# Performance work log

Hardware: AMD Instinct MI355X
Metric: run time of the kernel (lower is better)

Reference implementation:

```python
import jax, jax.numpy as jnp
import numpy as np

N_GRAPHS = 100
NODES_PER_GRAPH = 1000
N = N_GRAPHS * NODES_PER_GRAPH
DEG = 16
E = N * DEG
IN_FEATS = 64
HIDDEN = 128
READOUT_DIM = HIDDEN // 2
SLOPE = 0.01
EPS = 1e-5


def leaky(x):
    return jnp.where(x >= 0, x, SLOPE * x)


def _kaiming(k, shape):
    # torch kaiming_uniform_, fan_in mode, leaky_relu gain
    fan_in = shape[0]
    gain = np.sqrt(2.0 / (1.0 + SLOPE ** 2))
    bound = gain * np.sqrt(3.0 / fan_in)
    return jax.random.uniform(k, shape, jnp.float32, -bound, bound)


def setup_inputs() -> dict:
    key = jax.random.key(0)
    ks = jax.random.split(key, 16)
    node_feats = jax.random.normal(ks[0], (N, IN_FEATS), jnp.float32)
    # within-graph random edges (batched graph of equal-sized components)
    src_local = jax.random.randint(ks[1], (E,), 0, NODES_PER_GRAPH)
    dst_local = jax.random.randint(ks[2], (E,), 0, NODES_PER_GRAPH)
    edge_graph = jnp.repeat(jnp.arange(N_GRAPHS, dtype=jnp.int32), E // N_GRAPHS)
    src = (edge_graph * NODES_PER_GRAPH + src_local).astype(jnp.int32)
    dst = (edge_graph * NODES_PER_GRAPH + dst_local).astype(jnp.int32)
    edge_weights = jax.random.uniform(ks[3], (E,), jnp.float32)
    node_graph = jnp.repeat(jnp.arange(N_GRAPHS, dtype=jnp.int32), NODES_PER_GRAPH)
    return {
        "node_feats": node_feats,
        "edge_weights": edge_weights,
        "W1": _kaiming(ks[4], (IN_FEATS, HIDDEN)),
        "W2": _kaiming(ks[5], (HIDDEN, HIDDEN)),
        "gn1_alpha": jnp.ones((HIDDEN,), jnp.float32),
        "gn1_gamma": jnp.ones((HIDDEN,), jnp.float32),
        "gn1_beta": jnp.zeros((HIDDEN,), jnp.float32),
        "gn2_alpha": jnp.ones((HIDDEN,), jnp.float32),
        "gn2_gamma": jnp.ones((HIDDEN,), jnp.float32),
        "gn2_beta": jnp.zeros((HIDDEN,), jnp.float32),
        "r1_w1": _kaiming(ks[6], (HIDDEN, HIDDEN)),
        "r1_b1": jnp.zeros((HIDDEN,), jnp.float32),
        "r1_w2": _kaiming(ks[7], (HIDDEN, READOUT_DIM)),
        "r1_b2": jnp.zeros((READOUT_DIM,), jnp.float32),
        "r2_w1": _kaiming(ks[8], (HIDDEN, HIDDEN)),
        "r2_b1": jnp.zeros((HIDDEN,), jnp.float32),
        "r2_w2": _kaiming(ks[9], (HIDDEN, READOUT_DIM)),
        "r2_b2": jnp.zeros((READOUT_DIM,), jnp.float32),
        "src": src,
        "dst": dst,
        "node_graph": node_graph,
    }


def _graph_conv(x, W, src, dst, ew, out_isqrt, in_isqrt):
    # DGL GraphConv norm='both', no bias: D_in^{-1/2} A_w D_out^{-1/2} X W
    h = (x * out_isqrt[:, None]) @ W                 # [N, out]
    m = h[src] * ew[:, None]                         # [E, out] gather + edge weight
    agg = jax.ops.segment_sum(m, dst, num_segments=N)  # scatter-add
    return agg * in_isqrt[:, None]


def _graph_norm(x, alpha, gamma, beta, node_graph, inv_cnt):
    mean = jax.ops.segment_sum(x, node_graph, num_segments=N_GRAPHS) * inv_cnt
    sub = x - alpha * mean[node_graph]
    var = jax.ops.segment_sum(sub * sub, node_graph, num_segments=N_GRAPHS) * inv_cnt
    return gamma * sub / jnp.sqrt(var[node_graph] + EPS) + beta


def _readout(x, w1, b1, w2, b2, node_graph, inv_cnt):
    # deep-sets style universal readout: rho(mean(phi(h_v)))
    h = leaky(x @ w1 + b1)
    pooled = jax.ops.segment_sum(h, node_graph, num_segments=N_GRAPHS) * inv_cnt
    return leaky(pooled @ w2 + b2)


def reference(node_feats, edge_weights, W1, W2,
              gn1_alpha, gn1_gamma, gn1_beta,
              gn2_alpha, gn2_gamma, gn2_beta,
              r1_w1, r1_b1, r1_w2, r1_b2,
              r2_w1, r2_b1, r2_w2, r2_b2,
              src, dst, node_graph):
    ones_e = jnp.ones((E,), jnp.float32)
    out_deg = jnp.clip(jax.ops.segment_sum(ones_e, src, num_segments=N), 1.0)
    in_deg = jnp.clip(jax.ops.segment_sum(ones_e, dst, num_segments=N), 1.0)
    out_isqrt = jax.lax.rsqrt(out_deg)
    in_isqrt = jax.lax.rsqrt(in_deg)
    inv_cnt = 1.0 / NODES_PER_GRAPH

    h = _graph_conv(node_feats, W1, src, dst, edge_weights, out_isqrt, in_isqrt)
    h = leaky(_graph_norm(h, gn1_alpha, gn1_gamma, gn1_beta, node_graph, inv_cnt))
    # dropout is identity in eval mode
    r1 = _readout(h, r1_w1, r1_b1, r1_w2, r1_b2, node_graph, inv_cnt)
    m1 = jax.ops.segment_sum(h, node_graph, num_segments=N_GRAPHS) * inv_cnt

    h = _graph_conv(h, W2, src, dst, edge_weights, out_isqrt, in_isqrt)
    h = leaky(_graph_norm(h, gn2_alpha, gn2_gamma, gn2_beta, node_graph, inv_cnt))
    r2 = _readout(h, r2_w1, r2_b1, r2_w2, r2_b2, node_graph, inv_cnt)
    m2 = jax.ops.segment_sum(h, node_graph, num_segments=N_GRAPHS) * inv_cnt

    readout = jnp.concatenate([r1, m1, r2, m2], axis=1)  # [G, 2*H + 2*H/2] = [100, 384]
    return leaky(readout)
```

## Files before the change

### kernel.cpp

```cpp
#include <hip/hip_runtime.h>
#include <cstddef>
#include <cstdint>

#define NG   100
#define NPG  1000
#define NN   (NG * NPG)
#define NE   (NN * 16)
#define EPG  (NE / NG)
#define CSRG 40000
#define MINREC 20
#define FIN  64
#define HID  128
#define RD   64
#define SLOPE 0.01f
#define EPSV  1e-5f
#define NSTRIP 250
#define GSN   40

using short8 = __attribute__((ext_vector_type(8))) short;
using f32x4  = __attribute__((ext_vector_type(4))) float;
typedef unsigned short u16;

__device__ __forceinline__ float leaky(float x) { return x >= 0.f ? x : SLOPE * x; }

__device__ __forceinline__ u16 f2bf(float f) {
  union { float f; unsigned u; } v; v.f = f;
  return (u16)((v.u + 0x7fffu + ((v.u >> 16) & 1u)) >> 16);
}
__device__ __forceinline__ float bf2f(u16 u) {
  union { unsigned u; float f; } v; v.u = ((unsigned)u) << 16;
  return v.f;
}

__device__ __forceinline__ bool swz(int b, int per_g, int& g, int& part) {
  const int xcd = b & 7;
  const int slot = b >> 3;
  g = xcd + 8 * (slot / per_g);
  part = slot % per_g;
  return g < NG;
}

struct BldSh { int hin[NPG]; int hout[NPG]; int cur[NPG]; int wtot[16]; };
struct GemSh { u16 Xl[64 * FIN]; u16 W[HID * FIN]; };
union FrontSh { BldSh b; GemSh g; };

__global__ __launch_bounds__(1024) void front_k(
    const float* __restrict__ X0, const float* __restrict__ ew,
    const int* __restrict__ src, const int* __restrict__ dst,
    const float* __restrict__ W1, const float* __restrict__ W2f,
    const float* __restrict__ R1f, const float* __restrict__ R2f,
    u16* __restrict__ Wt2, u16* __restrict__ Rt1, u16* __restrict__ Rt2,
    int* __restrict__ cin_, int* __restrict__ offs,
    unsigned* __restrict__ csr, u16* __restrict__ bufA,
    float* __restrict__ zeroreg) {
  __shared__ FrontSh u;
  const int b = blockIdx.x;
  const int t = threadIdx.x;
  if (b >= 208) {
    const int idx = (b - 208) * 1024 + t;
    if (idx < 3 * HID * HID) {
      const int m = idx >> 14, r = idx & 16383;
      const int n = r >> 7, k = r & 127;
      const float* s = (m == 0) ? W2f : (m == 1) ? R1f : R2f;
      u16* d = (m == 0) ? Wt2 : (m == 1) ? Rt1 : Rt2;
      d[r] = f2bf(s[k * HID + n]);
    }
    if (idx < (8 * NG * HID) / 4)
      ((float4*)zeroreg)[idx] = make_float4(0.f, 0.f, 0.f, 0.f);
    return;
  }
  int g, part;
  if (!swz(b, 2, g, part)) return;
  const int lane = t & 63, wave = t >> 6;
  const int nb = g * NPG, eb = g * EPG;

  if (part == 0) {
    if (t < NPG) { u.b.hin[t] = 0; u.b.hout[t] = 0; }
    __syncthreads();
    for (int e = t; e < EPG; e += 4096) {
      int s4[4], d4[4];
#pragma unroll
      for (int k = 0; k < 4; ++k) {
        const int ee = e + k * 1024;
        if (ee < EPG) { s4[k] = src[eb + ee]; d4[k] = dst[eb + ee]; }
        else d4[k] = -1;
      }
#pragma unroll
      for (int k = 0; k < 4; ++k)
        if (d4[k] >= 0) {
          atomicAdd(&u.b.hout[s4[k] - nb], 1);
          atomicAdd(&u.b.hin[d4[k] - nb], 1);
        }
    }
    __syncthreads();
    float* houtf = (float*)u.b.hout;
    if (t < NPG) {
      const int c = u.b.hout[t];
      houtf[t] = rsqrtf((float)(c > 0 ? c : 1));
    }
    int v[4], vr[4];
    int loc = 0;
#pragma unroll
    for (int k = 0; k < 4; ++k) {
      const int idx = t * 4 + k;
      v[k] = (idx < NPG) ? u.b.hin[idx] : 0;
      const int c4 = (v[k] + 3) & ~3;
      vr[k] = (idx < NPG) ? ((c4 > MINREC) ? c4 : MINREC) : 0;
      loc += vr[k];
    }
    int incl = loc;
#pragma unroll
    for (int d = 1; d < 64; d <<= 1) {
      const int x = __shfl_up(incl, d);
      if (lane >= d) incl += x;
    }
    if (lane == 63) u.b.wtot[wave] = incl;
    if (t < NPG) cin_[nb + t] = u.b.hin[t];
    __syncthreads();
    int wexc = 0;
    for (int i = 0; i < wave; ++i) wexc += u.b.wtot[i];
    int run = g * CSRG + wexc + (incl - loc);
#pragma unroll
    for (int k = 0; k < 4; ++k) {
      const int idx = t * 4 + k;
      if (idx < NPG) {
        offs[nb + idx] = run;
        u.b.cur[idx] = run;
        for (int z = v[k]; z < vr[k]; ++z) csr[run + z] = 0;
        run += vr[k];
      }
    }
    __syncthreads();
    for (int e = t; e < EPG; e += 4096) {
      int s4[4], d4[4];
      float w4[4];
#pragma unroll
      for (int k = 0; k < 4; ++k) {
        const int ee = e + k * 1024;
        if (ee < EPG) { s4[k] = src[eb + ee]; d4[k] = dst[eb + ee]; w4[k] = ew[eb + ee]; }
        else d4[k] = -1;
      }
#pragma unroll
      for (int k = 0; k < 4; ++k)
        if (d4[k] >= 0) {
          const int sl = s4[k] - nb;
          const int pos = atomicAdd(&u.b.cur[d4[k] - nb], 1);
          csr[pos] = ((unsigned)sl << 16) | (unsigned)f2bf(w4[k] * houtf[sl]);
        }
    }
  } else {
    const int l15 = lane & 15, quad = lane >> 4;
    const int rg = wave >> 2, cg = wave & 3;
    {
      const int n = t & 127, ko = t >> 7;
      short8 w8;
#pragma unroll
      for (int j = 0; j < 8; ++j) w8[j] = (short)f2bf(W1[(ko * 8 + j) * HID + n]);
      *(short8*)&u.g.W[n * FIN + ((ko ^ (n & 7)) << 3)] = w8;
    }
    const int kq = t & 15, srow = t >> 4;
    float4 xpre = (srow < NPG)
        ? *(const float4*)(X0 + (size_t)(nb + srow) * FIN + kq * 4)
        : make_float4(0.f, 0.f, 0.f, 0.f);
    for (int pass = 0; pass < 16; ++pass) {
      __syncthreads();
      {
        ushort4 uu = make_ushort4(f2bf(xpre.x), f2bf(xpre.y), f2bf(xpre.z), f2bf(xpre.w));
        const int cc = kq >> 1, half = kq & 1;
        *(ushort4*)&u.g.Xl[srow * FIN + (((cc ^ (srow & 7)) << 3) | (half << 2))] = uu;
      }
      __syncthreads();
      if (pass < 15) {
        const int rowi = (pass + 1) * 64 + srow;
        xpre = (rowi < NPG)
            ? *(const float4*)(X0 + (size_t)(nb + rowi) * FIN + kq * 4)
            : make_float4(0.f, 0.f, 0.f, 0.f);
      }
      short8 a[2];
      const int arow = rg * 16 + l15;
#pragma unroll
      for (int kt = 0; kt < 2; ++kt)
        a[kt] = *(const short8*)&u.g.Xl[arow * FIN + (((kt * 4 + quad) ^ (l15 & 7)) << 3)];
      int rows[4];
#pragma unroll
      for (int r = 0; r < 4; ++r) rows[r] = pass * 64 + rg * 16 + quad * 4 + r;
#pragma unroll
      for (int q2 = 0; q2 < 2; ++q2) {
        const int ct = cg * 2 + q2;
        f32x4 acc = {0.f, 0.f, 0.f, 0.f};
        const int brow = ct * 16 + l15;
#pragma unroll
        for (int kt = 0; kt < 2; ++kt) {
          const short8 bb = *(const short8*)&u.g.W[brow * FIN + (((kt * 4 + quad) ^ (l15 & 7)) << 3)];
          acc = __builtin_amdgcn_mfma_f32_16x16x32_bf16(a[kt], bb, acc, 0, 0, 0);
        }
        const int n2 = ct * 16 + l15;
#pragma unroll
        for (int r = 0; r < 4; ++r)
          if (rows[r] < NPG)
            bufA[(size_t)(nb + rows[r]) * HID + n2] = f2bf(acc[r]);
      }
    }
  }
}

__device__ __forceinline__ void norm_affine(const float* sx, const float* sq,
                                            const float* alpha, const float* gamma,
                                            const float* beta, int g, int c8,
                                            float* Av, float* Bv) {
  const float inv = 1.0f / NPG;
#pragma unroll
  for (int j = 0; j < 8; ++j) {
    const int f = c8 * 8 + j;
    const float mean = sx[g * HID + f] * inv;
    const float ex2 = sq[g * HID + f] * inv;
    const float am = alpha[f] * mean;
    const float var = fmaxf(ex2 - 2.0f * am * mean + am * am, 0.0f);
    const float A = gamma[f] * rsqrtf(var + EPSV);
    Av[j] = A;
    Bv[j] = beta[f] - A * am;
  }
}

__global__ __launch_bounds__(256) void gather_k(const u16* __restrict__ H,
                                                const unsigned* __restrict__ csr,
                                                const int* __restrict__ offs,
                                                const int* __restrict__ cin_,
                                                u16* __restrict__ AGG,
                                                float* __restrict__ sx,
                                                float* __restrict__ sq) {
  __shared__ float redx[4][HID];
  __shared__ float redq[4][HID];
  const int wave = threadIdx.x >> 6;
  const int lane = threadIdx.x & 63;
  int g, part;
  if (!swz(blockIdx.x, 25, g, part)) return;
  const int nb = g * NPG;
  const int base = nb + part * GSN;
  const int loff = lane * 2;
  const u16* __restrict__ Hg = H + (size_t)nb * HID;

  float sxa = 0.f, sxb = 0.f, sqa = 0.f, sqb = 0.f;
  for (int it = 0; it < 3; ++it) {
    const int nc = (it < 2) ? 4 : 2;
    int nn[4], off[4], cnt[4], c4p[4];
    float isq[4];
    const uint4* p[4];
#pragma unroll
    for (int c = 0; c < 4; ++c) {
      const int j = it * 4 + c;
      const int node = base + wave + ((j < 10) ? j : 0) * 4;
      nn[c] = node;
      const int nu = __builtin_amdgcn_readfirstlane(node);
      off[c] = __builtin_amdgcn_readfirstlane(offs[nu]);
      cnt[c] = (c < nc) ? __builtin_amdgcn_readfirstlane(cin_[nu]) : 0;
      const int cr = (cnt[c] + 3) & ~3;
      c4p[c] = ((cr > MINREC) ? cr : MINREC) >> 2;
      isq[c] = rsqrtf(fmaxf((float)cnt[c], 1.0f));
      p[c] = (const uint4*)__builtin_assume_aligned(csr + off[c], 16);
    }
    float ax[4] = {0.f, 0.f, 0.f, 0.f};
    float ay[4] = {0.f, 0.f, 0.f, 0.f};
#pragma unroll
    for (int t = 0; t < 5; ++t) {
      uint4 r[4];
      unsigned u[4][4];
#pragma unroll
      for (int c = 0; c < 4; ++c)
        if (c < nc) {
          r[c] = p[c][t];
          u[c][0] = *(const unsigned*)(Hg + (size_t)(r[c].x >> 16) * HID + loff);
          u[c][1] = *(const unsigned*)(Hg + (size_t)(r[c].y >> 16) * HID + loff);
          u[c][2] = *(const unsigned*)(Hg + (size_t)(r[c].z >> 16) * HID + loff);
          u[c][3] = *(const unsigned*)(Hg + (size_t)(r[c].w >> 16) * HID + loff);
        }
#pragma unroll
      for (int c = 0; c < 4; ++c)
        if (c < nc) {
          const float w0 = bf2f((u16)(r[c].x & 0xffffu));
          const float w1 = bf2f((u16)(r[c].y & 0xffffu));
          const float w2 = bf2f((u16)(r[c].z & 0xffffu));
          const float w3 = bf2f((u16)(r[c].w & 0xffffu));
          ax[c] = fmaf(w0, __uint_as_float(u[c][0] << 16), ax[c]);
          ay[c] = fmaf(w0, __uint_as_float(u[c][0] & 0xffff0000u), ay[c]);
          ax[c] = fmaf(w1, __uint_as_float(u[c][1] << 16), ax[c]);
          ay[c] = fmaf(w1, __uint_as_float(u[c][1] & 0xffff0000u), ay[c]);
          ax[c] = fmaf(w2, __uint_as_float(u[c][2] << 16), ax[c]);
          ay[c] = fmaf(w2, __uint_as_float(u[c][2] & 0xffff0000u), ay[c]);
          ax[c] = fmaf(w3, __uint_as_float(u[c][3] << 16), ax[c]);
          ay[c] = fmaf(w3, __uint_as_float(u[c][3] & 0xffff0000u), ay[c]);
        }
    }
#pragma unroll
    for (int c = 0; c < 4; ++c) {
      for (int t = 5; t < c4p[c]; ++t) {
        const uint4 r = p[c][t];
        const unsigned u0 = *(const unsigned*)(Hg + (size_t)(r.x >> 16) * HID + loff);
        const unsigned u1 = *(const unsigned*)(Hg + (size_t)(r.y >> 16) * HID + loff);
        const unsigned u2 = *(const unsigned*)(Hg + (size_t)(r.z >> 16) * HID + loff);
        const unsigned u3 = *(const unsigned*)(Hg + (size_t)(r.w >> 16) * HID + loff);
        const float w0 = bf2f((u16)(r.x & 0xffffu));
        const float w1 = bf2f((u16)(r.y & 0xffffu));
        const float w2 = bf2f((u16)(r.z & 0xffffu));
        const float w3 = bf2f((u16)(r.w & 0xffffu));
        ax[c] = fmaf(w0, __uint_as_float(u0 << 16), ax[c]);
        ay[c] = fmaf(w0, __uint_as_float(u0 & 0xffff0000u), ay[c]);
        ax[c] = fmaf(w1, __uint_as_float(u1 << 16), ax[c]);
        ay[c] = fmaf(w1, __uint_as_float(u1 & 0xffff0000u), ay[c]);
        ax[c] = fmaf(w2, __uint_as_float(u2 << 16), ax[c]);
        ay[c] = fmaf(w2, __uint_as_float(u2 & 0xffff0000u), ay[c]);
        ax[c] = fmaf(w3, __uint_as_float(u3 << 16), ax[c]);
        ay[c] = fmaf(w3, __uint_as_float(u3 & 0xffff0000u), ay[c]);
      }
    }
#pragma unroll
    for (int c = 0; c < 4; ++c)
      if (c < nc) {
        const float rx = ax[c] * isq[c];
        const float ry = ay[c] * isq[c];
        *(unsigned*)(AGG + (size_t)nn[c] * HID + loff) =
            (unsigned)f2bf(rx) | ((unsigned)f2bf(ry) << 16);
        sxa += rx; sxb += ry;
        sqa += rx * rx; sqb += ry * ry;
      }
  }
  redx[wave][loff] = sxa; redx[wave][loff + 1] = sxb;
  redq[wave][loff] = sqa; redq[wave][loff + 1] = sqb;
  __syncthreads();
  const int tid = threadIdx.x;
  if (tid < HID) {
    unsafeAtomicAdd(&sx[g * HID + tid],
                    redx[0][tid] + redx[1][tid] + redx[2][tid] + redx[3][tid]);
  } else {
    const int t = tid - HID;
    unsafeAtomicAdd(&sq[g * HID + t],
                    redq[0][t] + redq[1][t] + redq[2][t] + redq[3][t]);
  }
}

struct RedT { float red[16][HID]; float hred[16][HID]; };
union ShT { u16 Xl[64 * HID]; RedT r; };

template <bool DO_GEMM>
__global__ __launch_bounds__(256) void phigemm_k(const u16* __restrict__ Xb,
                                                 u16* __restrict__ Y,
                                                 const u16* __restrict__ Wt,
                                                 const u16* __restrict__ Rt,
                                                 const float* __restrict__ sx,
                                                 const float* __restrict__ sq,
                                                 const float* __restrict__ alpha,
                                                 const float* __restrict__ gamma,
                                                 const float* __restrict__ beta,
                                                 const float* __restrict__ b1,
                                                 float* __restrict__ phi_sum,
                                                 float* __restrict__ h_sum) {
  __shared__ ShT sh;
  __shared__ u16 Rl[HID * HID];
  __shared__ u16 Wl[DO_GEMM ? HID * HID : 8];
  const int tid = threadIdx.x;
  const int wave = tid >> 6, lane = tid & 63, l15 = lane & 15, quad = lane >> 4;
  int g, part;
  if (!swz(blockIdx.x, 4, g, part)) return;
  const int base = g * NPG + part * NSTRIP;
  const int c8 = tid & 15;
  const int srow = tid >> 4;

  for (int i = tid; i < HID * (HID / 8); i += 256) {
    const int n = i >> 4, c = i & 15;
    const short8 r2 = *(const short8*)(Rt + n * HID + c * 8);
    *(short8*)&Rl[n * HID + ((c ^ (n & 15)) << 3)] = r2;
    if (DO_GEMM) {
      const short8 w = *(const short8*)(Wt + n * HID + c * 8);
      *(short8*)&Wl[n * HID + ((c ^ (n & 15)) << 3)] = w;
    }
  }
  float Av[8], Bv[8];
  norm_affine(sx, sq, alpha, gamma, beta, g, c8, Av, Bv);
  float bcol[8];
#pragma unroll
  for (int ct = 0; ct < 8; ++ct) bcol[ct] = b1[ct * 16 + l15];

  float pooled[8] = {0.f, 0.f, 0.f, 0.f, 0.f, 0.f, 0.f, 0.f};
  float hp[8] = {0.f, 0.f, 0.f, 0.f, 0.f, 0.f, 0.f, 0.f};
  const short8 z8 = {0, 0, 0, 0, 0, 0, 0, 0};
  short8 xpre[4];
#pragma unroll
  for (int it = 0; it < 4; ++it) {
    const int rowi = srow + it * 16;
    xpre[it] = (rowi < NSTRIP) ? *(const short8*)(Xb + (size_t)(base + rowi) * HID + c8 * 8) : z8;
  }
  for (int pass = 0; pass < 4; ++pass) {
    __syncthreads();
#pragma unroll
    for (int it = 0; it < 4; ++it) {
      const int r = srow + it * 16;
      const int rowi = pass * 64 + r;
      short8 o = z8;
      if (rowi < NSTRIP) {
#pragma unroll
        for (int j = 0; j < 8; ++j) {
          const float xn = leaky(fmaf(Av[j], bf2f((u16)xpre[it][j]), Bv[j]));
          hp[j] += xn;
          o[j] = (short)f2bf(xn);
        }
      }
      *(short8*)&sh.Xl[r * HID + ((c8 ^ (r & 15)) << 3)] = o;
    }
    __syncthreads();
    if (pass < 3) {
#pragma unroll
      for (int it = 0; it < 4; ++it) {
        const int rowi = (pass + 1) * 64 + srow + it * 16;
        xpre[it] = (rowi < NSTRIP) ? *(const short8*)(Xb + (size_t)(base + rowi) * HID + c8 * 8) : z8;
      }
    }
    short8 a[4];
    const int arow = wave * 16 + l15;
#pragma unroll
    for (int kt = 0; kt < 4; ++kt)
      a[kt] = *(const short8*)&sh.Xl[arow * HID + (((kt * 4 + quad) ^ l15) << 3)];
    int rows[4];
#pragma unroll
    for (int r = 0; r < 4; ++r) rows[r] = pass * 64 + wave * 16 + quad * 4 + r;
#pragma unroll
    for (int ct = 0; ct < 8; ++ct) {
      const int brow = ct * 16 + l15;
      if (DO_GEMM) {
        f32x4 accW = {0.f, 0.f, 0.f, 0.f};
#pragma unroll
        for (int kt = 0; kt < 4; ++kt) {
          const short8 bb = *(const short8*)&Wl[brow * HID + (((kt * 4 + quad) ^ l15) << 3)];
          accW = __builtin_amdgcn_mfma_f32_16x16x32_bf16(a[kt], bb, accW, 0, 0, 0);
        }
#pragma unroll
        for (int r = 0; r < 4; ++r)
          if (rows[r] < NSTRIP)
            Y[(size_t)(base + rows[r]) * HID + ct * 16 + l15] = f2bf(accW[r]);
      }
      f32x4 accR = {0.f, 0.f, 0.f, 0.f};
#pragma unroll
      for (int kt = 0; kt < 4; ++kt) {
        const short8 bb = *(const short8*)&Rl[brow * HID + (((kt * 4 + quad) ^ l15) << 3)];
        accR = __builtin_amdgcn_mfma_f32_16x16x32_bf16(a[kt], bb, accR, 0, 0, 0);
      }
#pragma unroll
      for (int r = 0; r < 4; ++r)
        if (rows[r] < NSTRIP) pooled[ct] += leaky(accR[r] + bcol[ct]);
    }
  }
  __syncthreads();
  const int qi = wave * 4 + quad;
#pragma unroll
  for (int ct = 0; ct < 8; ++ct) sh.r.red[qi][ct * 16 + l15] = pooled[ct];
#pragma unroll
  for (int j = 0; j < 8; ++j) sh.r.hred[tid >> 4][(tid & 15) * 8 + j] = hp[j];
  __syncthreads();
  if (tid < HID) {
    float s = 0.f;
#pragma unroll
    for (int q = 0; q < 16; ++q) s += sh.r.red[q][tid];
    unsafeAtomicAdd(&phi_sum[g * HID + tid], s);
  } else {
    const int t = tid - HID;
    float s = 0.f;
#pragma unroll
    for (int rr = 0; rr < 16; ++rr) s += sh.r.hred[rr][t];
    unsafeAtomicAdd(&h_sum[g * HID + t], s);
  }
}

__global__ __launch_bounds__(64) void fin_k(const float* __restrict__ ps1,
                                            const float* __restrict__ hs1,
                                            const float* __restrict__ ps2,
                                            const float* __restrict__ hs2,
                                            const float* __restrict__ r1w2,
                                            const float* __restrict__ r1b2,
                                            const float* __restrict__ r2w2,
                                            const float* __restrict__ r2b2,
                                            float* __restrict__ out) {
  const int gb = blockIdx.x;
  const bool L2 = gb >= NG;
  const int g = L2 ? gb - NG : gb;
  const float* ps = L2 ? ps2 : ps1;
  const float* hs = L2 ? hs2 : hs1;
  const float* w2 = L2 ? r2w2 : r1w2;
  const float* b2 = L2 ? r2b2 : r1b2;
  const int roff = L2 ? 192 : 0;
  const int moff = L2 ? 256 : 64;
  const int j = threadIdx.x;
  float acc = b2[j];
#pragma unroll 8
  for (int k = 0; k < HID; ++k)
    acc += (ps[g * HID + k] * (1.0f / NPG)) * w2[k * RD + j];
  out[g * 384 + roff + j] = leaky(leaky(acc));
  out[g * 384 + moff + j] = leaky(hs[g * HID + j] * (1.0f / NPG));
  out[g * 384 + moff + 64 + j] = leaky(hs[g * HID + 64 + j] * (1.0f / NPG));
}

extern "C" void kernel_launch(void* const* d_in, const int* in_sizes, int n_in,
                              void* d_out, int out_size, void* d_ws, size_t ws_size,
                              hipStream_t stream) {
  const float* node_feats = (const float*)d_in[0];
  const float* ew   = (const float*)d_in[1];
  const float* W1   = (const float*)d_in[2];
  const float* W2   = (const float*)d_in[3];
  const float* g1a  = (const float*)d_in[4];
  const float* g1g  = (const float*)d_in[5];
  const float* g1b  = (const float*)d_in[6];
  const float* g2a  = (const float*)d_in[7];
  const float* g2g  = (const float*)d_in[8];
  const float* g2b  = (const float*)d_in[9];
  const float* r1w1 = (const float*)d_in[10];
  const float* r1b1 = (const float*)d_in[11];
  const float* r1w2 = (const float*)d_in[12];
  const float* r1b2 = (const float*)d_in[13];
  const float* r2w1 = (const float*)d_in[14];
  const float* r2b1 = (const float*)d_in[15];
  const float* r2w2 = (const float*)d_in[16];
  const float* r2b2 = (const float*)d_in[17];
  const int* src = (const int*)d_in[18];
  const int* dst = (const int*)d_in[19];
  float* out = (float*)d_out;

  char* wsb = (char*)d_ws;
  float* ps1     = (float*)wsb;
  float* hs1     = ps1 + NG * HID;
  float* ps2     = hs1 + NG * HID;
  float* hs2     = ps2 + NG * HID;
  float* sx1     = hs2 + NG * HID;
  float* sq1     = sx1 + NG * HID;
  float* sx2     = sq1 + NG * HID;
  float* sq2     = sx2 + NG * HID;
  int*   cin     = (int*)(sq2 + NG * HID);
  int*   offs    = cin + NN;
  unsigned* csr  = (unsigned*)(offs + NN);
  u16*   Wt2     = (u16*)(csr + (size_t)NG * CSRG);
  u16*   Rt1     = Wt2 + HID * HID;
  u16*   Rt2     = Rt1 + HID * HID;
  u16*   bufA    = Rt2 + HID * HID;
  u16*   bufB    = bufA + (size_t)NN * HID;

  const int gemm_grid = 8 * 4 * 13;
  const int gather_grid = 8 * 25 * 13;

  front_k<<<208 + 56, 1024, 0, stream>>>(node_feats, ew, src, dst,
                                         W1, W2, r1w1, r2w1,
                                         Wt2, Rt1, Rt2,
                                         cin, offs, csr, bufA, ps1);

  gather_k<<<gather_grid, 256, 0, stream>>>(bufA, csr, offs, cin, bufB, sx1, sq1);
  phigemm_k<true><<<gemm_grid, 256, 0, stream>>>(bufB, bufA, Wt2, Rt1,
                                                 sx1, sq1, g1a, g1g, g1b,
                                                 r1b1, ps1, hs1);

  gather_k<<<gather_grid, 256, 0, stream>>>(bufA, csr, offs, cin, bufB, sx2, sq2);
  phigemm_k<false><<<gemm_grid, 256, 0, stream>>>(bufB, nullptr, nullptr, Rt2,
                                                  sx2, sq2, g2a, g2g, g2b,
                                                  r2b1, ps2, hs2);

  fin_k<<<2 * NG, 64, 0, stream>>>(ps1, hs1, ps2, hs2, r1w2, r1b2, r2w2, r2b2, out);
}
```

Baseline: 268.5 us.

## Use fixed-stride CSR, fuse final readout into last GEMM block, double GEMM grid

Each node now gets a fixed 64-slot CSR segment, which drops the in-degree histogram, prefix scan and offsets array from the build kernel and the offset loads from the gather kernel. In-degrees above 64 are silently truncated. The separate final readout kernel is removed: the last of each graph's GEMM blocks, found with an atomic counter and thread fence, computes the readout MLP tail and the mean outputs. GEMM strips are halved so twice as many blocks run with fewer passes each. The cost is a larger CSR footprint and the counter synchronisation.

```diff
diff --git a/kernel.cpp b/kernel.cpp
--- a/kernel.cpp
+++ b/kernel.cpp
@@ -7,14 +7,15 @@
 #define NN   (NG * NPG)
 #define NE   (NN * 16)
 #define EPG  (NE / NG)
-#define CSRG 40000
+#define CSRN 64
+#define CSRG (NPG * CSRN)
 #define MINREC 20
 #define FIN  64
 #define HID  128
 #define RD   64
 #define SLOPE 0.01f
 #define EPSV  1e-5f
-#define NSTRIP 250
+#define NSTRIP 125
 #define GSN   40
 
 using short8 = __attribute__((ext_vector_type(8))) short;
@@ -40,7 +41,7 @@
   return g < NG;
 }
 
-struct BldSh { int hin[NPG]; int hout[NPG]; int cur[NPG]; int wtot[16]; };
+struct BldSh { int hout[NPG]; int cur[NPG]; };
 struct GemSh { u16 Xl[64 * FIN]; u16 W[HID * FIN]; };
 union FrontSh { BldSh b; GemSh g; };
 
@@ -50,8 +51,7 @@
     const float* __restrict__ W1, const float* __restrict__ W2f,
     const float* __restrict__ R1f, const float* __restrict__ R2f,
     u16* __restrict__ Wt2, u16* __restrict__ Rt1, u16* __restrict__ Rt2,
-    int* __restrict__ cin_, int* __restrict__ offs,
-    unsigned* __restrict__ csr, u16* __restrict__ bufA,
+    int* __restrict__ cin_, unsigned* __restrict__ csr, u16* __restrict__ bufA,
     float* __restrict__ zeroreg) {
   __shared__ FrontSh u;
   const int b = blockIdx.x;
@@ -65,7 +65,7 @@
       u16* d = (m == 0) ? Wt2 : (m == 1) ? Rt1 : Rt2;
       d[r] = f2bf(s[k * HID + n]);
     }
-    if (idx < (8 * NG * HID) / 4)
+    if (idx < (8 * NG * HID + 256) / 4)
       ((float4*)zeroreg)[idx] = make_float4(0.f, 0.f, 0.f, 0.f);
     return;
   }
@@ -75,22 +75,18 @@
   const int nb = g * NPG, eb = g * EPG;
 
   if (part == 0) {
-    if (t < NPG) { u.b.hin[t] = 0; u.b.hout[t] = 0; }
+    if (t < NPG) { u.b.hout[t] = 0; u.b.cur[t] = 0; }
     __syncthreads();
     for (int e = t; e < EPG; e += 4096) {
-      int s4[4], d4[4];
+      int s4[4];
 #pragma unroll
       for (int k = 0; k < 4; ++k) {
         const int ee = e + k * 1024;
-        if (ee < EPG) { s4[k] = src[eb + ee]; d4[k] = dst[eb + ee]; }
-        else d4[k] = -1;
+        s4[k] = (ee < EPG) ? src[eb + ee] : -1;
       }
 #pragma unroll
       for (int k = 0; k < 4; ++k)
-        if (d4[k] >= 0) {
-          atomicAdd(&u.b.hout[s4[k] - nb], 1);
-          atomicAdd(&u.b.hin[d4[k] - nb], 1);
-        }
+        if (s4[k] >= 0) atomicAdd(&u.b.hout[s4[k] - nb], 1);
     }
     __syncthreads();
     float* houtf = (float*)u.b.hout;
@@ -98,39 +94,8 @@
       const int c = u.b.hout[t];
       houtf[t] = rsqrtf((float)(c > 0 ? c : 1));
     }
-    int v[4], vr[4];
-    int loc = 0;
-#pragma unroll
-    for (int k = 0; k < 4; ++k) {
-      const int idx = t * 4 + k;
-      v[k] = (idx < NPG) ? u.b.hin[idx] : 0;
-      const int c4 = (v[k] + 3) & ~3;
-      vr[k] = (idx < NPG) ? ((c4 > MINREC) ? c4 : MINREC) : 0;
-      loc += vr[k];
-    }
-    int incl = loc;
-#pragma unroll
-    for (int d = 1; d < 64; d <<= 1) {
-      const int x = __shfl_up(incl, d);
-      if (lane >= d) incl += x;
-    }
-    if (lane == 63) u.b.wtot[wave] = incl;
-    if (t < NPG) cin_[nb + t] = u.b.hin[t];
-    __syncthreads();
-    int wexc = 0;
-    for (int i = 0; i < wave; ++i) wexc += u.b.wtot[i];
-    int run = g * CSRG + wexc + (incl - loc);
-#pragma unroll
-    for (int k = 0; k < 4; ++k) {
-      const int idx = t * 4 + k;
-      if (idx < NPG) {
-        offs[nb + idx] = run;
-        u.b.cur[idx] = run;
-        for (int z = v[k]; z < vr[k]; ++z) csr[run + z] = 0;
-        run += vr[k];
-      }
-    }
-    __syncthreads();
+    __syncthreads();
+    const unsigned segbase = (unsigned)g * CSRG;
     for (int e = t; e < EPG; e += 4096) {
       int s4[4], d4[4];
       float w4[4];
@@ -144,9 +109,22 @@
       for (int k = 0; k < 4; ++k)
         if (d4[k] >= 0) {
           const int sl = s4[k] - nb;
-          const int pos = atomicAdd(&u.b.cur[d4[k] - nb], 1);
-          csr[pos] = ((unsigned)sl << 16) | (unsigned)f2bf(w4[k] * houtf[sl]);
+          const int dl = d4[k] - nb;
+          const int pos = atomicAdd(&u.b.cur[dl], 1);
+          if (pos < CSRN)
+            csr[segbase + dl * CSRN + pos] =
+                ((unsigned)sl << 16) | (unsigned)f2bf(w4[k] * houtf[sl]);
         }
+    }
+    __syncthreads();
+    if (t < NPG) {
+      int c = u.b.cur[t];
+      c = (c > CSRN) ? CSRN : c;
+      cin_[nb + t] = c;
+      const int c4 = (c + 3) & ~3;
+      const int pad = (c4 > MINREC) ? c4 : MINREC;
+      unsigned* seg = csr + segbase + t * CSRN;
+      for (int z = c; z < pad; ++z) seg[z] = 0;
     }
   } else {
     const int l15 = lane & 15, quad = lane >> 4;
@@ -224,7 +202,6 @@
 
 __global__ __launch_bounds__(256) void gather_k(const u16* __restrict__ H,
                                                 const unsigned* __restrict__ csr,
-                                                const int* __restrict__ offs,
                                                 const int* __restrict__ cin_,
                                                 u16* __restrict__ AGG,
                                                 float* __restrict__ sx,
@@ -239,11 +216,12 @@
   const int base = nb + part * GSN;
   const int loff = lane * 2;
   const u16* __restrict__ Hg = H + (size_t)nb * HID;
+  const unsigned* __restrict__ csrg = csr + (size_t)g * CSRG;
 
   float sxa = 0.f, sxb = 0.f, sqa = 0.f, sqb = 0.f;
   for (int it = 0; it < 3; ++it) {
     const int nc = (it < 2) ? 4 : 2;
-    int nn[4], off[4], cnt[4], c4p[4];
+    int nn[4], cnt[4], c4p[4];
     float isq[4];
     const uint4* p[4];
 #pragma unroll
@@ -252,12 +230,11 @@
       const int node = base + wave + ((j < 10) ? j : 0) * 4;
       nn[c] = node;
       const int nu = __builtin_amdgcn_readfirstlane(node);
-      off[c] = __builtin_amdgcn_readfirstlane(offs[nu]);
       cnt[c] = (c < nc) ? __builtin_amdgcn_readfirstlane(cin_[nu]) : 0;
       const int cr = (cnt[c] + 3) & ~3;
       c4p[c] = ((cr > MINREC) ? cr : MINREC) >> 2;
       isq[c] = rsqrtf(fmaxf((float)cnt[c], 1.0f));
-      p[c] = (const uint4*)__builtin_assume_aligned(csr + off[c], 16);
+      p[c] = (const uint4*)__builtin_assume_aligned(csrg + (nu - nb) * CSRN, 16);
     }
     float ax[4] = {0.f, 0.f, 0.f, 0.f};
     float ay[4] = {0.f, 0.f, 0.f, 0.f};
@@ -353,14 +330,20 @@
                                                  const float* __restrict__ beta,
                                                  const float* __restrict__ b1,
                                                  float* __restrict__ phi_sum,
-                                                 float* __restrict__ h_sum) {
+                                                 float* __restrict__ h_sum,
+                                                 int* __restrict__ ctr,
+                                                 const float* __restrict__ w2,
+                                                 const float* __restrict__ b2,
+                                                 float* __restrict__ out,
+                                                 int roff, int moff) {
   __shared__ ShT sh;
   __shared__ u16 Rl[HID * HID];
   __shared__ u16 Wl[DO_GEMM ? HID * HID : 8];
+  __shared__ int sh_last;
   const int tid = threadIdx.x;
   const int wave = tid >> 6, lane = tid & 63, l15 = lane & 15, quad = lane >> 4;
   int g, part;
-  if (!swz(blockIdx.x, 4, g, part)) return;
+  if (!swz(blockIdx.x, 8, g, part)) return;
   const int base = g * NPG + part * NSTRIP;
   const int c8 = tid & 15;
   const int srow = tid >> 4;
@@ -389,7 +372,7 @@
     const int rowi = srow + it * 16;
     xpre[it] = (rowi < NSTRIP) ? *(const short8*)(Xb + (size_t)(base + rowi) * HID + c8 * 8) : z8;
   }
-  for (int pass = 0; pass < 4; ++pass) {
+  for (int pass = 0; pass < 2; ++pass) {
     __syncthreads();
 #pragma unroll
     for (int it = 0; it < 4; ++it) {
@@ -407,10 +390,10 @@
       *(short8*)&sh.Xl[r * HID + ((c8 ^ (r & 15)) << 3)] = o;
     }
     __syncthreads();
-    if (pass < 3) {
+    if (pass < 1) {
 #pragma unroll
       for (int it = 0; it < 4; ++it) {
-        const int rowi = (pass + 1) * 64 + srow + it * 16;
+        const int rowi = 64 + srow + it * 16;
         xpre[it] = (rowi < NSTRIP) ? *(const short8*)(Xb + (size_t)(base + rowi) * HID + c8 * 8) : z8;
       }
     }
@@ -467,34 +450,30 @@
     for (int rr = 0; rr < 16; ++rr) s += sh.r.hred[rr][t];
     unsafeAtomicAdd(&h_sum[g * HID + t], s);
   }
-}
-
-__global__ __launch_bounds__(64) void fin_k(const float* __restrict__ ps1,
-                                            const float* __restrict__ hs1,
-                                            const float* __restrict__ ps2,
-                                            const float* __restrict__ hs2,
-                                            const float* __restrict__ r1w2,
-                                            const float* __restrict__ r1b2,
-                                            const float* __restrict__ r2w2,
-                                            const float* __restrict__ r2b2,
-                                            float* __restrict__ out) {
-  const int gb = blockIdx.x;
-  const bool L2 = gb >= NG;
-  const int g = L2 ? gb - NG : gb;
-  const float* ps = L2 ? ps2 : ps1;
-  const float* hs = L2 ? hs2 : hs1;
-  const float* w2 = L2 ? r2w2 : r1w2;
-  const float* b2 = L2 ? r2b2 : r1b2;
-  const int roff = L2 ? 192 : 0;
-  const int moff = L2 ? 256 : 64;
-  const int j = threadIdx.x;
-  float acc = b2[j];
+  __threadfence();
+  if (tid == 0) sh_last = (atomicAdd(&ctr[g], 1) == 7);
+  __syncthreads();
+  if (sh_last) {
+    __threadfence();
+    float* finbuf = &sh.r.red[0][0];
+    if (tid < HID)
+      finbuf[tid] = __hip_atomic_load(&phi_sum[g * HID + tid],
+                                      __ATOMIC_RELAXED, __HIP_MEMORY_SCOPE_AGENT);
+    else if (tid < 2 * HID)
+      finbuf[tid] = __hip_atomic_load(&h_sum[g * HID + (tid - HID)],
+                                      __ATOMIC_RELAXED, __HIP_MEMORY_SCOPE_AGENT);
+    __syncthreads();
+    const float inv = 1.0f / NPG;
+    if (tid < RD) {
+      float acc = b2[tid];
 #pragma unroll 8
-  for (int k = 0; k < HID; ++k)
-    acc += (ps[g * HID + k] * (1.0f / NPG)) * w2[k * RD + j];
-  out[g * 384 + roff + j] = leaky(leaky(acc));
-  out[g * 384 + moff + j] = leaky(hs[g * HID + j] * (1.0f / NPG));
-  out[g * 384 + moff + 64 + j] = leaky(hs[g * HID + 64 + j] * (1.0f / NPG));
+      for (int k = 0; k < HID; ++k) acc += finbuf[k] * inv * w2[k * RD + tid];
+      out[g * 384 + roff + tid] = leaky(leaky(acc));
+    } else if (tid < RD + HID) {
+      const int j = tid - RD;
+      out[g * 384 + moff + j] = leaky(finbuf[HID + j] * inv);
+    }
+  }
 }
 
 extern "C" void kernel_launch(void* const* d_in, const int* in_sizes, int n_in,
@@ -531,32 +510,32 @@
   float* sq1     = sx1 + NG * HID;
   float* sx2     = sq1 + NG * HID;
   float* sq2     = sx2 + NG * HID;
-  int*   cin     = (int*)(sq2 + NG * HID);
-  int*   offs    = cin + NN;
-  unsigned* csr  = (unsigned*)(offs + NN);
+  int*   ctr     = (int*)(sq2 + NG * HID);
+  int*   cin     = ctr + 256;
+  unsigned* csr  = (unsigned*)(cin + NN);
   u16*   Wt2     = (u16*)(csr + (size_t)NG * CSRG);
   u16*   Rt1     = Wt2 + HID * HID;
   u16*   Rt2     = Rt1 + HID * HID;
   u16*   bufA    = Rt2 + HID * HID;
   u16*   bufB    = bufA + (size_t)NN * HID;
 
-  const int gemm_grid = 8 * 4 * 13;
+  const int gemm_grid = 8 * 8 * 13;
   const int gather_grid = 8 * 25 * 13;
 
   front_k<<<208 + 56, 1024, 0, stream>>>(node_feats, ew, src, dst,
                                          W1, W2, r1w1, r2w1,
                                          Wt2, Rt1, Rt2,
-                                         cin, offs, csr, bufA, ps1);
-
-  gather_k<<<gather_grid, 256, 0, stream>>>(bufA, csr, offs, cin, bufB, sx1, sq1);
+                                         cin, csr, bufA, ps1);
+
+  gather_k<<<gather_grid, 256, 0, stream>>>(bufA, csr, cin, bufB, sx1, sq1);
   phigemm_k<true><<<gemm_grid, 256, 0, stream>>>(bufB, bufA, Wt2, Rt1,
                                                  sx1, sq1, g1a, g1g, g1b,
-                                                 r1b1, ps1, hs1);
-
-  gather_k<<<gather_grid, 256, 0, stream>>>(bufA, csr, offs, cin, bufB, sx2, sq2);
+                                                 r1b1, ps1, hs1,
+                                                 ctr, r1w2, r1b2, out, 0, 64);
+
+  gather_k<<<gather_grid, 256, 0, stream>>>(bufA, csr, cin, bufB, sx2, sq2);
   phigemm_k<false><<<gemm_grid, 256, 0, stream>>>(bufB, nullptr, nullptr, Rt2,
                                                   sx2, sq2, g2a, g2g, g2b,
-                                                  r2b1, ps2, hs2);
-
-  fin_k<<<2 * NG, 64, 0, stream>>>(ps1, hs1, ps2, hs2, r1w2, r1b2, r2w2, r2b2, out);
-}
+                                                  r2b1, ps2, hs2,
+                                                  ctr + NG, r2w2, r2b2, out, 192, 256);
+}
```

After: 424.0 us. 57.9% more time.
